# Optimization experiments

Measured on AMD Instinct MI355X. Metric: run time of the kernel, lower is better.

Reference implementation:

```python
import jax, jax.numpy as jnp
import numpy as np

N_BALL = 256
N_EDGES = N_BALL * (N_BALL - 1)  # fully connected, no self loops
BATCH = 4
F_IN = 64
H = 64  # out_channels
EDGE_TYPES = 2


def _edge_structure():
    # receiver repeated pattern / sender covering all other nodes, as in NRI
    recv, send = [], []
    for r in range(N_BALL):
        for s in range(N_BALL):
            if s != r:
                recv.append(r)
                send.append(s)
    eye = np.eye(N_BALL, dtype=np.float32)
    rel_rec = eye[np.array(recv)]   # [E, N]
    rel_send = eye[np.array(send)]  # [E, N]
    return jnp.asarray(rel_rec), jnp.asarray(rel_send)


def setup_inputs() -> dict:
    key = jax.random.key(0)
    ks = jax.random.split(key, 12)
    rel_rec, rel_send = _edge_structure()
    s1 = 1.0 / np.sqrt(2 * F_IN)
    s2 = 1.0 / np.sqrt(H)
    s3 = 1.0 / np.sqrt(F_IN + H)
    return {
        "inputs": jax.random.normal(ks[0], (BATCH, N_BALL, F_IN), jnp.float32),
        "rel_type": jax.random.uniform(ks[1], (BATCH, N_EDGES, EDGE_TYPES), jnp.float32),
        "rel_rec": rel_rec,
        "rel_send": rel_send,
        # per-edge-type message MLPs (stacked over edge types)
        "W1": jax.random.uniform(ks[2], (EDGE_TYPES, 2 * F_IN, H), jnp.float32, -s1, s1),
        "b1": jax.random.uniform(ks[3], (EDGE_TYPES, H), jnp.float32, -s1, s1),
        "W2": jax.random.uniform(ks[4], (EDGE_TYPES, H, H), jnp.float32, -s2, s2),
        "b2": jax.random.uniform(ks[5], (EDGE_TYPES, H), jnp.float32, -s2, s2),
        # output MLP
        "Wo1": jax.random.uniform(ks[6], (F_IN + H, H), jnp.float32, -s3, s3),
        "bo1": jax.random.uniform(ks[7], (H,), jnp.float32, -s3, s3),
        "Wo2": jax.random.uniform(ks[8], (H, H), jnp.float32, -s2, s2),
        "bo2": jax.random.uniform(ks[9], (H,), jnp.float32, -s2, s2),
    }


def reference(inputs, rel_type, rel_rec, rel_send, W1, b1, W2, b2, Wo1, bo1, Wo2, bo2):
    # gather node features onto edges via one-hot matmuls
    receivers = jnp.einsum('en,bnf->bef', rel_rec, inputs)   # [B,E,F]
    senders = jnp.einsum('en,bnf->bef', rel_send, inputs)    # [B,E,F]
    pre_msg = jnp.concatenate([senders, receivers], axis=-1)  # [B,E,2F]

    all_msgs = jnp.zeros(pre_msg.shape[:2] + (H,), dtype=pre_msg.dtype)
    for i in range(EDGE_TYPES):  # skip_first=False -> start at 0
        msg = jax.nn.relu(pre_msg @ W1[i] + b1[i])
        msg = jax.nn.relu(msg @ W2[i] + b2[i])
        all_msgs = all_msgs + msg * rel_type[:, :, i:i + 1]

    # scatter-aggregate edge messages back to receiver nodes
    agg_msgs = jnp.einsum('beh,en->bnh', all_msgs, rel_rec)   # [B,N,H]
    aug_inputs = jnp.concatenate([inputs, agg_msgs], axis=-1)  # [B,N,F+H]

    pred = jax.nn.relu(aug_inputs @ Wo1 + bo1)
    pred = jax.nn.relu(pred @ Wo2 + bo2)
    return inputs + pred
```

## Files before the change

### kernel.cpp

```cpp
#include <hip/hip_runtime.h>
#include <hip/hip_bf16.h>

#define BATCH 4
#define NB    256
#define NE    (NB*(NB-1))

typedef short    short8 __attribute__((ext_vector_type(8)));
typedef float    f32x16 __attribute__((ext_vector_type(16)));

static __device__ __forceinline__ short f2bf(float x) {
    return __builtin_bit_cast(short, __float2bfloat16(x));
}
static __device__ __forceinline__ float bf2f(short s) {
    unsigned u = ((unsigned)(unsigned short)s) << 16;
    return __builtin_bit_cast(float, u);
}
static __device__ __forceinline__ f32x16 splat16(float v) {
    f32x16 r;
    #pragma unroll
    for (int e = 0; e < 16; ++e) r[e] = v;
    return r;
}

#define MFMA(C, A, B) C = __builtin_amdgcn_mfma_f32_32x32x16_bf16(A, B, C, 0, 0, 0)

#define MK_BW(dst, BASE, K0, NT) do {                                          \
    const float* _p = W1l + (BASE) + (16*(K0) + 8*lh) * 64 + l31 + 32*(NT);    \
    short8 _v;                                                                 \
    _v[0]=f2bf(_p[0]);   _v[1]=f2bf(_p[64]);  _v[2]=f2bf(_p[128]);             \
    _v[3]=f2bf(_p[192]); _v[4]=f2bf(_p[256]); _v[5]=f2bf(_p[320]);             \
    _v[6]=f2bf(_p[384]); _v[7]=f2bf(_p[448]);                                  \
    (dst) = _v; } while (0)

__global__ __launch_bounds__(256) void prep_kernel(
    const float* __restrict__ x,
    const float* __restrict__ W1,
    const float* __restrict__ b1,
    const float* __restrict__ W2,
    short* __restrict__ Pbf,
    float* __restrict__ Qg,
    short* __restrict__ W2f)
{
    const int t    = threadIdx.x;
    const int lane = t & 63;
    const int w    = t >> 6;
    const int l31  = lane & 31;
    const int lh   = lane >> 5;
    const int blk  = blockIdx.x;

    __shared__ __align__(16) float W1l[8192];
    __shared__ __align__(16) short xbf[8192];

    if (blk < 16) {
        const int i    = blk >> 3;
        const int b    = (blk >> 1) & 3;
        const int half = blk & 1;
        const int n0   = half * 128;
        const int ibb  = i * 4 + b;
        const float* xb = x + (size_t)b * NB * 64;

        #pragma unroll
        for (int q = 0; q < 8; ++q) {
            const int e = (q * 256 + t) * 4;
            *(float4*)(W1l + e) = *(const float4*)(W1 + (size_t)i * 8192 + e);
        }
        #pragma unroll
        for (int rep = 0; rep < 2; ++rep) {
            const int n  = (t >> 2) + 64 * rep;
            const int f0 = (t & 3) * 16;
            const float* src = xb + (n0 + n) * 64 + f0;
            float4 v0 = *(const float4*)(src);
            float4 v1 = *(const float4*)(src + 4);
            float4 v2 = *(const float4*)(src + 8);
            float4 v3 = *(const float4*)(src + 12);
            short8 s0 = { f2bf(v0.x), f2bf(v0.y), f2bf(v0.z), f2bf(v0.w),
                          f2bf(v1.x), f2bf(v1.y), f2bf(v1.z), f2bf(v1.w) };
            short8 s1 = { f2bf(v2.x), f2bf(v2.y), f2bf(v2.z), f2bf(v2.w),
                          f2bf(v3.x), f2bf(v3.y), f2bf(v3.z), f2bf(v3.w) };
            const int sw = (n & 7) << 4;
            *(short8*)((char*)xbf + n * 128 + ((f0 * 2)      ^ sw)) = s0;
            *(short8*)((char*)xbf + n * 128 + ((f0 * 2 + 16) ^ sw)) = s1;
        }
        __syncthreads();

        const int rloc = 32 * w + l31;
        const int swr  = (rloc & 7) << 4;
        const short8 XB0 = *(const short8*)((const char*)xbf + rloc*128 + ((16*lh)       ^ swr));
        const short8 XB1 = *(const short8*)((const char*)xbf + rloc*128 + ((32 + 16*lh)  ^ swr));
        const short8 XB2 = *(const short8*)((const char*)xbf + rloc*128 + ((64 + 16*lh)  ^ swr));
        const short8 XB3 = *(const short8*)((const char*)xbf + rloc*128 + ((96 + 16*lh)  ^ swr));

        {
            short8 B0, B1, B2, B3;
            MK_BW(B0, 0, 0, 0); MK_BW(B1, 0, 1, 0); MK_BW(B2, 0, 2, 0); MK_BW(B3, 0, 3, 0);
            f32x16 c = splat16(0.f);
            MFMA(c, XB0, B0); MFMA(c, XB1, B1); MFMA(c, XB2, B2); MFMA(c, XB3, B3);
            #pragma unroll
            for (int rg = 0; rg < 16; ++rg) {
                const int nn = n0 + 32*w + (rg & 3) + 8*(rg >> 2) + 4*lh;
                Pbf[(size_t)ibb*16384 + (l31 >> 3)*2048 + nn*8 + (l31 & 7)] = f2bf(c[rg]);
            }
        }
        {
            short8 B0, B1, B2, B3;
            MK_BW(B0, 0, 0, 1); MK_BW(B1, 0, 1, 1); MK_BW(B2, 0, 2, 1); MK_BW(B3, 0, 3, 1);
            f32x16 c = splat16(0.f);
            MFMA(c, XB0, B0); MFMA(c, XB1, B1); MFMA(c, XB2, B2); MFMA(c, XB3, B3);
            #pragma unroll
            for (int rg = 0; rg < 16; ++rg) {
                const int nn = n0 + 32*w + (rg & 3) + 8*(rg >> 2) + 4*lh;
                Pbf[(size_t)ibb*16384 + (4 + (l31 >> 3))*2048 + nn*8 + (l31 & 7)] = f2bf(c[rg]);
            }
        }
        {
            short8 B0, B1, B2, B3;
            MK_BW(B0, 4096, 0, 0); MK_BW(B1, 4096, 1, 0); MK_BW(B2, 4096, 2, 0); MK_BW(B3, 4096, 3, 0);
            f32x16 c = splat16(0.f);
            MFMA(c, XB0, B0); MFMA(c, XB1, B1); MFMA(c, XB2, B2); MFMA(c, XB3, B3);
            const float b1v = b1[i * 64 + l31];
            #pragma unroll
            for (int rg = 0; rg < 16; ++rg) {
                const int nn = n0 + 32*w + (rg & 3) + 8*(rg >> 2) + 4*lh;
                Qg[(size_t)ibb*16384 + nn*64 + l31] = c[rg] + b1v;
            }
        }
        {
            short8 B0, B1, B2, B3;
            MK_BW(B0, 4096, 0, 1); MK_BW(B1, 4096, 1, 1); MK_BW(B2, 4096, 2, 1); MK_BW(B3, 4096, 3, 1);
            f32x16 c = splat16(0.f);
            MFMA(c, XB0, B0); MFMA(c, XB1, B1); MFMA(c, XB2, B2); MFMA(c, XB3, B3);
            const float b1v = b1[i * 64 + 32 + l31];
            #pragma unroll
            for (int rg = 0; rg < 16; ++rg) {
                const int nn = n0 + 32*w + (rg & 3) + 8*(rg >> 2) + 4*lh;
                Qg[(size_t)ibb*16384 + nn*64 + 32 + l31] = c[rg] + b1v;
            }
        }
    } else {
        #pragma unroll
        for (int q = 0; q < 32; ++q) {
            const int e = q * 256 + t;
            const int i = e >> 12, k = (e >> 6) & 63, n = e & 63;
            const float v = W2[e];
            const int k0 = k >> 4, j = k & 7, hm = (k >> 3) & 1;
            const int nt = n >> 5;
            W2f[(((i*2 + nt)*4 + k0)*64 + hm*32 + (n & 31))*8 + j] = f2bf(v);
        }
    }
}


#define MK_A2(dst, PV, I, K0) do {                                             \
    float4 _q0 = *(const float4*)(&qrow[I][16*(K0) + 8*lh]);                   \
    float4 _q1 = *(const float4*)(&qrow[I][16*(K0) + 8*lh + 4]);               \
    short8 _v;                                                                 \
    _v[0] = f2bf(fmaxf(bf2f((PV)[0]) + _q0.x, 0.f));                           \
    _v[1] = f2bf(fmaxf(bf2f((PV)[1]) + _q0.y, 0.f));                           \
    _v[2] = f2bf(fmaxf(bf2f((PV)[2]) + _q0.z, 0.f));                           \
    _v[3] = f2bf(fmaxf(bf2f((PV)[3]) + _q0.w, 0.f));                           \
    _v[4] = f2bf(fmaxf(bf2f((PV)[4]) + _q1.x, 0.f));                           \
    _v[5] = f2bf(fmaxf(bf2f((PV)[5]) + _q1.y, 0.f));                           \
    _v[6] = f2bf(fmaxf(bf2f((PV)[6]) + _q1.z, 0.f));                           \
    _v[7] = f2bf(fmaxf(bf2f((PV)[7]) + _q1.w, 0.f));                           \
    (dst) = _v; } while (0)

#define EPI_Q(C, PS, I, ET, QD) do {                                           \
    float4 _rq = *(const float4*)(&rt2[I][64*w + 32*(ET) + 8*(QD) + 4*lh]);    \
    PS += fmaxf((C)[4*(QD)],   0.f) * _rq.x;                                   \
    PS += fmaxf((C)[4*(QD)+1], 0.f) * _rq.y;                                   \
    PS += fmaxf((C)[4*(QD)+2], 0.f) * _rq.z;                                   \
    PS += fmaxf((C)[4*(QD)+3], 0.f) * _rq.w; } while (0)

#define TILE2(I, ET, PA, PB, PC, PD, BVA, BVB) do {                            \
    short8 _a0, _a1, _a2, _a3;                                                 \
    MK_A2(_a0, PA, I, 0); MK_A2(_a1, PB, I, 1);                                \
    MK_A2(_a2, PC, I, 2); MK_A2(_a3, PD, I, 3);                                \
    {                                                                          \
        f32x16 _c = splat16(BVA);                                              \
        MFMA(_c, _a0, *(const short8*)(W2l + (((I)*8 + 0)*64 + lane)*8));      \
        MFMA(_c, _a1, *(const short8*)(W2l + (((I)*8 + 1)*64 + lane)*8));      \
        MFMA(_c, _a2, *(const short8*)(W2l + (((I)*8 + 2)*64 + lane)*8));      \
        MFMA(_c, _a3, *(const short8*)(W2l + (((I)*8 + 3)*64 + lane)*8));      \
        EPI_Q(_c, psum0, I, ET, 0); EPI_Q(_c, psum0, I, ET, 1);                \
        EPI_Q(_c, psum0, I, ET, 2); EPI_Q(_c, psum0, I, ET, 3);                \
    }                                                                          \
    {                                                                          \
        f32x16 _c = splat16(BVB);                                              \
        MFMA(_c, _a0, *(const short8*)(W2l + (((I)*8 + 4)*64 + lane)*8));      \
        MFMA(_c, _a1, *(const short8*)(W2l + (((I)*8 + 5)*64 + lane)*8));      \
        MFMA(_c, _a2, *(const short8*)(W2l + (((I)*8 + 6)*64 + lane)*8));      \
        MFMA(_c, _a3, *(const short8*)(W2l + (((I)*8 + 7)*64 + lane)*8));      \
        EPI_Q(_c, psum1, I, ET, 0); EPI_Q(_c, psum1, I, ET, 1);                \
        EPI_Q(_c, psum1, I, ET, 2); EPI_Q(_c, psum1, I, ET, 3);                \
    } } while (0)

#define LD_P(I, K0, S) \
    (*(const short8*)(PbfG + ((size_t)((I)*4+b)*8 + 2*(K0)+lh)*2048 + (size_t)(S)*8))

__global__ __launch_bounds__(256, 3) void main_kernel(
    const float* __restrict__ x,
    const float* __restrict__ rel_type,
    const float* __restrict__ b2,
    const float* __restrict__ Wo1,
    const float* __restrict__ bo1,
    const float* __restrict__ Wo2,
    const float* __restrict__ bo2,
    const short* __restrict__ PbfG,
    const float* __restrict__ Qg,
    const short* __restrict__ W2fG,
    float* __restrict__ out)
{
    const int b    = blockIdx.x >> 8;
    const int r    = blockIdx.x & 255;
    const int t    = threadIdx.x;
    const int lane = t & 63;
    const int w    = t >> 6;
    const int l31  = lane & 31;
    const int lh   = lane >> 5;

    __shared__ __align__(16) short W2l[8192];
    __shared__ __align__(16) float rt2[2][256];
    __shared__ __align__(16) float qrow[2][64];
    __shared__ __align__(16) float red[4][64];
    __shared__ __align__(16) float xl[64];
    __shared__ __align__(16) float aggl[64];
    __shared__ __align__(16) float predl[64];

    const float* xb = x + (size_t)b * NB * 64;

    if (t < 255) {
        const float2 pv = *(const float2*)(rel_type + ((size_t)b * NE + (size_t)r * 255 + t) * 2);
        rt2[0][t] = pv.x;
        rt2[1][t] = pv.y;
    } else {
        rt2[0][255] = 0.f; rt2[1][255] = 0.f;
    }
    #pragma unroll
    for (int q = 0; q < 4; ++q) {
        const int e = (q * 256 + t) * 8;
        *(short8*)(W2l + e) = *(const short8*)(W2fG + e);
    }
    if (t < 128) {
        const int i = t >> 6, h = t & 63;
        qrow[i][h] = Qg[(size_t)(i * 4 + b) * 16384 + r * 64 + h];
    }
    if (t >= 192) xl[t - 192] = xb[r * 64 + (t - 192)];

    const int kap0 = 64 * w + l31;
    const int kap1 = kap0 + 32;
    int s0 = (kap0 < r) ? kap0 : kap0 + 1; if (s0 > 255) s0 = 255;
    int s1 = (kap1 < r) ? kap1 : kap1 + 1; if (s1 > 255) s1 = 255;

    short8 P00 = LD_P(0,0,s0), P01 = LD_P(0,1,s0), P02 = LD_P(0,2,s0), P03 = LD_P(0,3,s0);

    const float bv00 = b2[l31],      bv01 = b2[32 + l31];
    const float bv10 = b2[64 + l31], bv11 = b2[96 + l31];

    __syncthreads();

    float psum0 = 0.f, psum1 = 0.f;

    short8 P10 = LD_P(0,0,s1), P11 = LD_P(0,1,s1), P12 = LD_P(0,2,s1), P13 = LD_P(0,3,s1);
    TILE2(0, 0, P00, P01, P02, P03, bv00, bv01);

    P00 = LD_P(1,0,s0); P01 = LD_P(1,1,s0); P02 = LD_P(1,2,s0); P03 = LD_P(1,3,s0);
    TILE2(0, 1, P10, P11, P12, P13, bv00, bv01);

    P10 = LD_P(1,0,s1); P11 = LD_P(1,1,s1); P12 = LD_P(1,2,s1); P13 = LD_P(1,3,s1);
    TILE2(1, 0, P00, P01, P02, P03, bv10, bv11);

    TILE2(1, 1, P10, P11, P12, P13, bv10, bv11);

    psum0 += __shfl_xor(psum0, 32, 64);
    psum1 += __shfl_xor(psum1, 32, 64);
    if (lh == 0) {
        red[w][l31]      = psum0;
        red[w][l31 + 32] = psum1;
    }
    __syncthreads();
    if (t < 64) aggl[t] = red[0][t] + red[1][t] + red[2][t] + red[3][t];
    __syncthreads();

    {
        const float* src = (w < 2) ? (xl + w * 32) : (aggl + (w - 2) * 32);
        const float* Wp  = Wo1 + (w * 32) * 64 + lane;
        float s = 0.f;
        #pragma unroll
        for (int jj = 0; jj < 32; ++jj) s = fmaf(src[jj], Wp[jj * 64], s);
        red[w][lane] = s;
    }
    __syncthreads();
    if (t < 64)
        predl[t] = fmaxf(red[0][t] + red[1][t] + red[2][t] + red[3][t] + bo1[t], 0.f);
    __syncthreads();

    {
        const float* Wp = Wo2 + (w * 16) * 64 + lane;
        float s = 0.f;
        #pragma unroll
        for (int jj = 0; jj < 16; ++jj) s = fmaf(predl[w * 16 + jj], Wp[jj * 64], s);
        red[w][lane] = s;
    }
    __syncthreads();
    if (t < 64)
        out[((size_t)b * NB + r) * 64 + t] =
            xl[t] + fmaxf(red[0][t] + red[1][t] + red[2][t] + red[3][t] + bo2[t], 0.f);
}

extern "C" void kernel_launch(void* const* d_in, const int* in_sizes, int n_in,
                              void* d_out, int out_size, void* d_ws, size_t ws_size,
                              hipStream_t stream) {
    (void)in_sizes; (void)n_in; (void)out_size; (void)ws_size;

    const float* x    = (const float*)d_in[0];
    const float* rt   = (const float*)d_in[1];
    const float* W1   = (const float*)d_in[4];
    const float* b1   = (const float*)d_in[5];
    const float* W2   = (const float*)d_in[6];
    const float* b2   = (const float*)d_in[7];
    const float* Wo1  = (const float*)d_in[8];
    const float* bo1  = (const float*)d_in[9];
    const float* Wo2  = (const float*)d_in[10];
    const float* bo2  = (const float*)d_in[11];
    float* out = (float*)d_out;

    char* ws = (char*)d_ws;
    short* Pbf = (short*)ws;
    float* Qg  = (float*)(ws + 262144);
    short* W2f = (short*)(ws + 786432);

    prep_kernel<<<17, 256, 0, stream>>>(x, W1, b1, W2, Pbf, Qg, W2f);
    main_kernel<<<BATCH * NB, 256, 0, stream>>>(x, rt, b2, Wo1, bo1, Wo2, bo2,
                                                Pbf, Qg, W2f, out);
}
```

Measured before the change: 22.51 us.

## Process two receiver rows per block to amortize W2 staging

Each block now handles two receiver nodes instead of one, halving the grid to 512 blocks. The W2 weight tile copy into LDS and the setup work are shared across both rows, and the first P loads for the second row are issued before the first row's epilogue. The cost is more serial work per block and fewer blocks to spread across CUs, which lowers parallelism on a 256-CU part.

```diff
diff --git a/kernel.cpp b/kernel.cpp
--- a/kernel.cpp
+++ b/kernel.cpp
@@ -150,9 +150,9 @@
 }
 
 
-#define MK_A2(dst, PV, I, K0) do {                                             \
-    float4 _q0 = *(const float4*)(&qrow[I][16*(K0) + 8*lh]);                   \
-    float4 _q1 = *(const float4*)(&qrow[I][16*(K0) + 8*lh + 4]);               \
+#define MK_A2(dst, PV, RR, I, K0) do {                                         \
+    float4 _q0 = *(const float4*)(&qrow[RR][I][16*(K0) + 8*lh]);               \
+    float4 _q1 = *(const float4*)(&qrow[RR][I][16*(K0) + 8*lh + 4]);           \
     short8 _v;                                                                 \
     _v[0] = f2bf(fmaxf(bf2f((PV)[0]) + _q0.x, 0.f));                           \
     _v[1] = f2bf(fmaxf(bf2f((PV)[1]) + _q0.y, 0.f));                           \
@@ -164,25 +164,25 @@
     _v[7] = f2bf(fmaxf(bf2f((PV)[7]) + _q1.w, 0.f));                           \
     (dst) = _v; } while (0)
 
-#define EPI_Q(C, PS, I, ET, QD) do {                                           \
-    float4 _rq = *(const float4*)(&rt2[I][64*w + 32*(ET) + 8*(QD) + 4*lh]);    \
+#define EPI_Q(C, PS, RR, I, ET, QD) do {                                       \
+    float4 _rq = *(const float4*)(&rt2[RR][I][64*w + 32*(ET) + 8*(QD) + 4*lh]);\
     PS += fmaxf((C)[4*(QD)],   0.f) * _rq.x;                                   \
     PS += fmaxf((C)[4*(QD)+1], 0.f) * _rq.y;                                   \
     PS += fmaxf((C)[4*(QD)+2], 0.f) * _rq.z;                                   \
     PS += fmaxf((C)[4*(QD)+3], 0.f) * _rq.w; } while (0)
 
-#define TILE2(I, ET, PA, PB, PC, PD, BVA, BVB) do {                            \
+#define TILE2(RR, I, ET, PA, PB, PC, PD, BVA, BVB, PS0, PS1) do {              \
     short8 _a0, _a1, _a2, _a3;                                                 \
-    MK_A2(_a0, PA, I, 0); MK_A2(_a1, PB, I, 1);                                \
-    MK_A2(_a2, PC, I, 2); MK_A2(_a3, PD, I, 3);                                \
+    MK_A2(_a0, PA, RR, I, 0); MK_A2(_a1, PB, RR, I, 1);                        \
+    MK_A2(_a2, PC, RR, I, 2); MK_A2(_a3, PD, RR, I, 3);                        \
     {                                                                          \
         f32x16 _c = splat16(BVA);                                              \
         MFMA(_c, _a0, *(const short8*)(W2l + (((I)*8 + 0)*64 + lane)*8));      \
         MFMA(_c, _a1, *(const short8*)(W2l + (((I)*8 + 1)*64 + lane)*8));      \
         MFMA(_c, _a2, *(const short8*)(W2l + (((I)*8 + 2)*64 + lane)*8));      \
         MFMA(_c, _a3, *(const short8*)(W2l + (((I)*8 + 3)*64 + lane)*8));      \
-        EPI_Q(_c, psum0, I, ET, 0); EPI_Q(_c, psum0, I, ET, 1);                \
-        EPI_Q(_c, psum0, I, ET, 2); EPI_Q(_c, psum0, I, ET, 3);                \
+        EPI_Q(_c, PS0, RR, I, ET, 0); EPI_Q(_c, PS0, RR, I, ET, 1);            \
+        EPI_Q(_c, PS0, RR, I, ET, 2); EPI_Q(_c, PS0, RR, I, ET, 3);            \
     }                                                                          \
     {                                                                          \
         f32x16 _c = splat16(BVB);                                              \
@@ -190,9 +190,46 @@
         MFMA(_c, _a1, *(const short8*)(W2l + (((I)*8 + 5)*64 + lane)*8));      \
         MFMA(_c, _a2, *(const short8*)(W2l + (((I)*8 + 6)*64 + lane)*8));      \
         MFMA(_c, _a3, *(const short8*)(W2l + (((I)*8 + 7)*64 + lane)*8));      \
-        EPI_Q(_c, psum1, I, ET, 0); EPI_Q(_c, psum1, I, ET, 1);                \
-        EPI_Q(_c, psum1, I, ET, 2); EPI_Q(_c, psum1, I, ET, 3);                \
+        EPI_Q(_c, PS1, RR, I, ET, 0); EPI_Q(_c, PS1, RR, I, ET, 1);            \
+        EPI_Q(_c, PS1, RR, I, ET, 2); EPI_Q(_c, PS1, RR, I, ET, 3);            \
     } } while (0)
+
+#define EPILOG(RR, PS0, PS1) do {                                              \
+    float _p0 = (PS0) + __shfl_xor((PS0), 32, 64);                             \
+    float _p1 = (PS1) + __shfl_xor((PS1), 32, 64);                             \
+    if (lh == 0) {                                                             \
+        red[w][l31]      = _p0;                                                \
+        red[w][l31 + 32] = _p1;                                                \
+    }                                                                          \
+    __syncthreads();                                                           \
+    if (t < 64) aggl[t] = red[0][t] + red[1][t] + red[2][t] + red[3][t];       \
+    __syncthreads();                                                           \
+    {                                                                          \
+        const float* _src = (w < 2) ? (&xl[RR][0] + w * 32)                    \
+                                    : (aggl + (w - 2) * 32);                   \
+        const float* _Wp  = Wo1 + (w * 32) * 64 + lane;                        \
+        float _s = 0.f;                                                        \
+        _Pragma("unroll")                                                      \
+        for (int _jj = 0; _jj < 32; ++_jj) _s = fmaf(_src[_jj], _Wp[_jj*64], _s);\
+        red[w][lane] = _s;                                                     \
+    }                                                                          \
+    __syncthreads();                                                           \
+    if (t < 64)                                                                \
+        predl[t] = fmaxf(red[0][t]+red[1][t]+red[2][t]+red[3][t]+bo1[t], 0.f); \
+    __syncthreads();                                                           \
+    {                                                                          \
+        const float* _Wp = Wo2 + (w * 16) * 64 + lane;                         \
+        float _s = 0.f;                                                        \
+        _Pragma("unroll")                                                      \
+        for (int _jj = 0; _jj < 16; ++_jj)                                     \
+            _s = fmaf(predl[w*16 + _jj], _Wp[_jj*64], _s);                     \
+        red[w][lane] = _s;                                                     \
+    }                                                                          \
+    __syncthreads();                                                           \
+    if (t < 64)                                                                \
+        out[((size_t)b * NB + rbase + (RR)) * 64 + t] =                        \
+            xl[RR][t] + fmaxf(red[0][t]+red[1][t]+red[2][t]+red[3][t]+bo2[t], 0.f);\
+    __syncthreads(); } while (0)
 
 #define LD_P(I, K0, S) \
     (*(const short8*)(PbfG + ((size_t)((I)*4+b)*8 + 2*(K0)+lh)*2048 + (size_t)(S)*8))
@@ -210,101 +247,89 @@
     const short* __restrict__ W2fG,
     float* __restrict__ out)
 {
-    const int b    = blockIdx.x >> 8;
-    const int r    = blockIdx.x & 255;
-    const int t    = threadIdx.x;
-    const int lane = t & 63;
-    const int w    = t >> 6;
-    const int l31  = lane & 31;
-    const int lh   = lane >> 5;
+    const int b     = blockIdx.x >> 7;
+    const int rbase = (blockIdx.x & 127) * 2;
+    const int t     = threadIdx.x;
+    const int lane  = t & 63;
+    const int w     = t >> 6;
+    const int l31   = lane & 31;
+    const int lh    = lane >> 5;
 
     __shared__ __align__(16) short W2l[8192];
-    __shared__ __align__(16) float rt2[2][256];
-    __shared__ __align__(16) float qrow[2][64];
+    __shared__ __align__(16) float rt2[2][2][256];
+    __shared__ __align__(16) float qrow[2][2][64];
     __shared__ __align__(16) float red[4][64];
-    __shared__ __align__(16) float xl[64];
+    __shared__ __align__(16) float xl[2][64];
     __shared__ __align__(16) float aggl[64];
     __shared__ __align__(16) float predl[64];
 
-    const float* xb = x + (size_t)b * NB * 64;
-
-    if (t < 255) {
-        const float2 pv = *(const float2*)(rel_type + ((size_t)b * NE + (size_t)r * 255 + t) * 2);
-        rt2[0][t] = pv.x;
-        rt2[1][t] = pv.y;
-    } else {
-        rt2[0][255] = 0.f; rt2[1][255] = 0.f;
+    #pragma unroll
+    for (int rr = 0; rr < 2; ++rr) {
+        if (t < 255) {
+            const float2 pv = *(const float2*)(rel_type +
+                ((size_t)b * NE + (size_t)(rbase + rr) * 255 + t) * 2);
+            rt2[rr][0][t] = pv.x;
+            rt2[rr][1][t] = pv.y;
+        } else {
+            rt2[rr][0][255] = 0.f; rt2[rr][1][255] = 0.f;
+        }
     }
     #pragma unroll
     for (int q = 0; q < 4; ++q) {
         const int e = (q * 256 + t) * 8;
         *(short8*)(W2l + e) = *(const short8*)(W2fG + e);
     }
-    if (t < 128) {
-        const int i = t >> 6, h = t & 63;
-        qrow[i][h] = Qg[(size_t)(i * 4 + b) * 16384 + r * 64 + h];
+    {
+        const int rr = t >> 7, i = (t >> 6) & 1, h = t & 63;
+        qrow[rr][i][h] = Qg[(size_t)(i * 4 + b) * 16384 + (rbase + rr) * 64 + h];
     }
-    if (t >= 192) xl[t - 192] = xb[r * 64 + (t - 192)];
+    if (t < 128) xl[t >> 6][t & 63] =
+        x[((size_t)b * NB + rbase + (t >> 6)) * 64 + (t & 63)];
 
     const int kap0 = 64 * w + l31;
     const int kap1 = kap0 + 32;
-    int s0 = (kap0 < r) ? kap0 : kap0 + 1; if (s0 > 255) s0 = 255;
-    int s1 = (kap1 < r) ? kap1 : kap1 + 1; if (s1 > 255) s1 = 255;
-
-    short8 P00 = LD_P(0,0,s0), P01 = LD_P(0,1,s0), P02 = LD_P(0,2,s0), P03 = LD_P(0,3,s0);
+    const int r0 = rbase, r1 = rbase + 1;
+    int s0a = (kap0 < r0) ? kap0 : kap0 + 1; if (s0a > 255) s0a = 255;
+    int s1a = (kap1 < r0) ? kap1 : kap1 + 1; if (s1a > 255) s1a = 255;
+    int s0b = (kap0 < r1) ? kap0 : kap0 + 1; if (s0b > 255) s0b = 255;
+    int s1b = (kap1 < r1) ? kap1 : kap1 + 1; if (s1b > 255) s1b = 255;
+
+    short8 P00 = LD_P(0,0,s0a), P01 = LD_P(0,1,s0a), P02 = LD_P(0,2,s0a), P03 = LD_P(0,3,s0a);
 
     const float bv00 = b2[l31],      bv01 = b2[32 + l31];
     const float bv10 = b2[64 + l31], bv11 = b2[96 + l31];
 
     __syncthreads();
 
-    float psum0 = 0.f, psum1 = 0.f;
-
-    short8 P10 = LD_P(0,0,s1), P11 = LD_P(0,1,s1), P12 = LD_P(0,2,s1), P13 = LD_P(0,3,s1);
-    TILE2(0, 0, P00, P01, P02, P03, bv00, bv01);
-
-    P00 = LD_P(1,0,s0); P01 = LD_P(1,1,s0); P02 = LD_P(1,2,s0); P03 = LD_P(1,3,s0);
-    TILE2(0, 1, P10, P11, P12, P13, bv00, bv01);
-
-    P10 = LD_P(1,0,s1); P11 = LD_P(1,1,s1); P12 = LD_P(1,2,s1); P13 = LD_P(1,3,s1);
-    TILE2(1, 0, P00, P01, P02, P03, bv10, bv11);
-
-    TILE2(1, 1, P10, P11, P12, P13, bv10, bv11);
-
-    psum0 += __shfl_xor(psum0, 32, 64);
-    psum1 += __shfl_xor(psum1, 32, 64);
-    if (lh == 0) {
-        red[w][l31]      = psum0;
-        red[w][l31 + 32] = psum1;
-    }
-    __syncthreads();
-    if (t < 64) aggl[t] = red[0][t] + red[1][t] + red[2][t] + red[3][t];
-    __syncthreads();
-
-    {
-        const float* src = (w < 2) ? (xl + w * 32) : (aggl + (w - 2) * 32);
-        const float* Wp  = Wo1 + (w * 32) * 64 + lane;
-        float s = 0.f;
-        #pragma unroll
-        for (int jj = 0; jj < 32; ++jj) s = fmaf(src[jj], Wp[jj * 64], s);
-        red[w][lane] = s;
-    }
-    __syncthreads();
-    if (t < 64)
-        predl[t] = fmaxf(red[0][t] + red[1][t] + red[2][t] + red[3][t] + bo1[t], 0.f);
-    __syncthreads();
-
-    {
-        const float* Wp = Wo2 + (w * 16) * 64 + lane;
-        float s = 0.f;
-        #pragma unroll
-        for (int jj = 0; jj < 16; ++jj) s = fmaf(predl[w * 16 + jj], Wp[jj * 64], s);
-        red[w][lane] = s;
-    }
-    __syncthreads();
-    if (t < 64)
-        out[((size_t)b * NB + r) * 64 + t] =
-            xl[t] + fmaxf(red[0][t] + red[1][t] + red[2][t] + red[3][t] + bo2[t], 0.f);
+    float psA0 = 0.f, psA1 = 0.f;
+
+    short8 P10 = LD_P(0,0,s1a), P11 = LD_P(0,1,s1a), P12 = LD_P(0,2,s1a), P13 = LD_P(0,3,s1a);
+    TILE2(0, 0, 0, P00, P01, P02, P03, bv00, bv01, psA0, psA1);
+
+    P00 = LD_P(1,0,s0a); P01 = LD_P(1,1,s0a); P02 = LD_P(1,2,s0a); P03 = LD_P(1,3,s0a);
+    TILE2(0, 0, 1, P10, P11, P12, P13, bv00, bv01, psA0, psA1);
+
+    P10 = LD_P(1,0,s1a); P11 = LD_P(1,1,s1a); P12 = LD_P(1,2,s1a); P13 = LD_P(1,3,s1a);
+    TILE2(0, 1, 0, P00, P01, P02, P03, bv10, bv11, psA0, psA1);
+    TILE2(0, 1, 1, P10, P11, P12, P13, bv10, bv11, psA0, psA1);
+
+    short8 N0 = LD_P(0,0,s0b), N1 = LD_P(0,1,s0b), N2 = LD_P(0,2,s0b), N3 = LD_P(0,3,s0b);
+
+    EPILOG(0, psA0, psA1);
+
+    float psB0 = 0.f, psB1 = 0.f;
+
+    short8 M0 = LD_P(0,0,s1b), M1 = LD_P(0,1,s1b), M2 = LD_P(0,2,s1b), M3 = LD_P(0,3,s1b);
+    TILE2(1, 0, 0, N0, N1, N2, N3, bv00, bv01, psB0, psB1);
+
+    N0 = LD_P(1,0,s0b); N1 = LD_P(1,1,s0b); N2 = LD_P(1,2,s0b); N3 = LD_P(1,3,s0b);
+    TILE2(1, 0, 1, M0, M1, M2, M3, bv00, bv01, psB0, psB1);
+
+    M0 = LD_P(1,0,s1b); M1 = LD_P(1,1,s1b); M2 = LD_P(1,2,s1b); M3 = LD_P(1,3,s1b);
+    TILE2(1, 1, 0, N0, N1, N2, N3, bv10, bv11, psB0, psB1);
+    TILE2(1, 1, 1, M0, M1, M2, M3, bv10, bv11, psB0, psB1);
+
+    EPILOG(1, psB0, psB1);
 }
 
 extern "C" void kernel_launch(void* const* d_in, const int* in_sizes, int n_in,
@@ -330,6 +355,6 @@
     short* W2f = (short*)(ws + 786432);
 
     prep_kernel<<<17, 256, 0, stream>>>(x, W1, b1, W2, Pbf, Qg, W2f);
-    main_kernel<<<BATCH * NB, 256, 0, stream>>>(x, rt, b2, Wo1, bo1, Wo2, bo2,
-                                                Pbf, Qg, W2f, out);
-}
+    main_kernel<<<512, 256, 0, stream>>>(x, rt, b2, Wo1, bo1, Wo2, bo2,
+                                         Pbf, Qg, W2f, out);
+}
```

New measurement: 43.43 us. 1.93x slower.

## Split prep kernel across 64 blocks, one MFMA tile per wave

Applied to the files above, without the earlier changes.

The prep kernel's node-projection phase now uses 64 blocks of 32 nodes instead of 16 blocks of 128 nodes. Each wave computes a single 32x32 output tile (P half or Q half) instead of four sequential tiles. The goal is to shorten the serial prep stage that runs before the main kernel by spreading it over more CUs. The cost is that each block reloads the 32KB W1 slice into LDS, which adds redundant global traffic.

```diff
diff --git a/kernel.cpp b/kernel.cpp
--- a/kernel.cpp
+++ b/kernel.cpp
@@ -49,91 +49,61 @@
     const int blk  = blockIdx.x;
 
     __shared__ __align__(16) float W1l[8192];
-    __shared__ __align__(16) short xbf[8192];
-
-    if (blk < 16) {
-        const int i    = blk >> 3;
-        const int b    = (blk >> 1) & 3;
-        const int half = blk & 1;
-        const int n0   = half * 128;
-        const int ibb  = i * 4 + b;
-        const float* xb = x + (size_t)b * NB * 64;
+    __shared__ __align__(16) short xbf[2048];
+
+    if (blk < 64) {
+        const int i   = blk >> 5;
+        const int rem = blk & 31;
+        const int bp  = rem >> 3;
+        const int n0  = (rem & 7) * 32;
+        const int ibb = i * 4 + bp;
+        const float* xb = x + (size_t)bp * NB * 64;
 
         #pragma unroll
         for (int q = 0; q < 8; ++q) {
             const int e = (q * 256 + t) * 4;
             *(float4*)(W1l + e) = *(const float4*)(W1 + (size_t)i * 8192 + e);
         }
-        #pragma unroll
-        for (int rep = 0; rep < 2; ++rep) {
-            const int n  = (t >> 2) + 64 * rep;
-            const int f0 = (t & 3) * 16;
-            const float* src = xb + (n0 + n) * 64 + f0;
+        {
+            const int row = t >> 3;
+            const int f0  = (t & 7) * 8;
+            const float* src = xb + (n0 + row) * 64 + f0;
             float4 v0 = *(const float4*)(src);
             float4 v1 = *(const float4*)(src + 4);
-            float4 v2 = *(const float4*)(src + 8);
-            float4 v3 = *(const float4*)(src + 12);
-            short8 s0 = { f2bf(v0.x), f2bf(v0.y), f2bf(v0.z), f2bf(v0.w),
-                          f2bf(v1.x), f2bf(v1.y), f2bf(v1.z), f2bf(v1.w) };
-            short8 s1 = { f2bf(v2.x), f2bf(v2.y), f2bf(v2.z), f2bf(v2.w),
-                          f2bf(v3.x), f2bf(v3.y), f2bf(v3.z), f2bf(v3.w) };
-            const int sw = (n & 7) << 4;
-            *(short8*)((char*)xbf + n * 128 + ((f0 * 2)      ^ sw)) = s0;
-            *(short8*)((char*)xbf + n * 128 + ((f0 * 2 + 16) ^ sw)) = s1;
+            short8 s = { f2bf(v0.x), f2bf(v0.y), f2bf(v0.z), f2bf(v0.w),
+                         f2bf(v1.x), f2bf(v1.y), f2bf(v1.z), f2bf(v1.w) };
+            const int sw = (row & 7) << 4;
+            *(short8*)((char*)xbf + row * 128 + ((f0 * 2) ^ sw)) = s;
         }
         __syncthreads();
 
-        const int rloc = 32 * w + l31;
-        const int swr  = (rloc & 7) << 4;
-        const short8 XB0 = *(const short8*)((const char*)xbf + rloc*128 + ((16*lh)       ^ swr));
-        const short8 XB1 = *(const short8*)((const char*)xbf + rloc*128 + ((32 + 16*lh)  ^ swr));
-        const short8 XB2 = *(const short8*)((const char*)xbf + rloc*128 + ((64 + 16*lh)  ^ swr));
-        const short8 XB3 = *(const short8*)((const char*)xbf + rloc*128 + ((96 + 16*lh)  ^ swr));
-
-        {
-            short8 B0, B1, B2, B3;
-            MK_BW(B0, 0, 0, 0); MK_BW(B1, 0, 1, 0); MK_BW(B2, 0, 2, 0); MK_BW(B3, 0, 3, 0);
-            f32x16 c = splat16(0.f);
-            MFMA(c, XB0, B0); MFMA(c, XB1, B1); MFMA(c, XB2, B2); MFMA(c, XB3, B3);
+        const int swr = (l31 & 7) << 4;
+        const short8 XB0 = *(const short8*)((const char*)xbf + l31*128 + ((16*lh)      ^ swr));
+        const short8 XB1 = *(const short8*)((const char*)xbf + l31*128 + ((32 + 16*lh) ^ swr));
+        const short8 XB2 = *(const short8*)((const char*)xbf + l31*128 + ((64 + 16*lh) ^ swr));
+        const short8 XB3 = *(const short8*)((const char*)xbf + l31*128 + ((96 + 16*lh) ^ swr));
+
+        const int base = (w < 2) ? 0 : 4096;
+        const int nt   = w & 1;
+        short8 B0, B1, B2, B3;
+        MK_BW(B0, base, 0, nt); MK_BW(B1, base, 1, nt);
+        MK_BW(B2, base, 2, nt); MK_BW(B3, base, 3, nt);
+        f32x16 c = splat16(0.f);
+        MFMA(c, XB0, B0); MFMA(c, XB1, B1); MFMA(c, XB2, B2); MFMA(c, XB3, B3);
+
+        if (w < 2) {
+            const int hh = l31 + 32 * nt;
             #pragma unroll
             for (int rg = 0; rg < 16; ++rg) {
-                const int nn = n0 + 32*w + (rg & 3) + 8*(rg >> 2) + 4*lh;
-                Pbf[(size_t)ibb*16384 + (l31 >> 3)*2048 + nn*8 + (l31 & 7)] = f2bf(c[rg]);
+                const int nn = n0 + (rg & 3) + 8 * (rg >> 2) + 4 * lh;
+                Pbf[(size_t)ibb * 16384 + (hh >> 3) * 2048 + nn * 8 + (hh & 7)] = f2bf(c[rg]);
             }
-        }
-        {
-            short8 B0, B1, B2, B3;
-            MK_BW(B0, 0, 0, 1); MK_BW(B1, 0, 1, 1); MK_BW(B2, 0, 2, 1); MK_BW(B3, 0, 3, 1);
-            f32x16 c = splat16(0.f);
-            MFMA(c, XB0, B0); MFMA(c, XB1, B1); MFMA(c, XB2, B2); MFMA(c, XB3, B3);
+        } else {
+            const float b1v = b1[i * 64 + 32 * nt + l31];
             #pragma unroll
             for (int rg = 0; rg < 16; ++rg) {
-                const int nn = n0 + 32*w + (rg & 3) + 8*(rg >> 2) + 4*lh;
-                Pbf[(size_t)ibb*16384 + (4 + (l31 >> 3))*2048 + nn*8 + (l31 & 7)] = f2bf(c[rg]);
-            }
-        }
-        {
-            short8 B0, B1, B2, B3;
-            MK_BW(B0, 4096, 0, 0); MK_BW(B1, 4096, 1, 0); MK_BW(B2, 4096, 2, 0); MK_BW(B3, 4096, 3, 0);
-            f32x16 c = splat16(0.f);
-            MFMA(c, XB0, B0); MFMA(c, XB1, B1); MFMA(c, XB2, B2); MFMA(c, XB3, B3);
-            const float b1v = b1[i * 64 + l31];
-            #pragma unroll
-            for (int rg = 0; rg < 16; ++rg) {
-                const int nn = n0 + 32*w + (rg & 3) + 8*(rg >> 2) + 4*lh;
-                Qg[(size_t)ibb*16384 + nn*64 + l31] = c[rg] + b1v;
-            }
-        }
-        {
-            short8 B0, B1, B2, B3;
-            MK_BW(B0, 4096, 0, 1); MK_BW(B1, 4096, 1, 1); MK_BW(B2, 4096, 2, 1); MK_BW(B3, 4096, 3, 1);
-            f32x16 c = splat16(0.f);
-            MFMA(c, XB0, B0); MFMA(c, XB1, B1); MFMA(c, XB2, B2); MFMA(c, XB3, B3);
-            const float b1v = b1[i * 64 + 32 + l31];
-            #pragma unroll
-            for (int rg = 0; rg < 16; ++rg) {
-                const int nn = n0 + 32*w + (rg & 3) + 8*(rg >> 2) + 4*lh;
-                Qg[(size_t)ibb*16384 + nn*64 + 32 + l31] = c[rg] + b1v;
+                const int nn = n0 + (rg & 3) + 8 * (rg >> 2) + 4 * lh;
+                Qg[(size_t)ibb * 16384 + nn * 64 + 32 * nt + l31] = c[rg] + b1v;
             }
         }
     } else {
@@ -329,7 +299,7 @@
     float* Qg  = (float*)(ws + 262144);
     short* W2f = (short*)(ws + 786432);
 
-    prep_kernel<<<17, 256, 0, stream>>>(x, W1, b1, W2, Pbf, Qg, W2f);
+    prep_kernel<<<65, 256, 0, stream>>>(x, W1, b1, W2, Pbf, Qg, W2f);
     main_kernel<<<BATCH * NB, 256, 0, stream>>>(x, rt, b2, Wo1, bo1, Wo2, bo2,
                                                 Pbf, Qg, W2f, out);
 }
```

Measured after the change: 22.68 us. About the same (+0.7%).
